# Optimization experiments

Measured on AMD Instinct MI355X. Metric: run time of the kernel, lower is better.

## Reference

```python
import jax, jax.numpy as jnp
import numpy as np

N_NODES = 50000
N_EDGES = 800000
EPS = 1e-5
NEG_SLOPE = 0.2


def _gatv2(x, src, dst, Wl, bl, Wr, br, att, bias, concat, N):
    # PyG GATv2Conv: xl = lin_l(x) (source side), xr = lin_r(x) (target side)
    H, C = att.shape
    xl = (x @ Wl + bl).reshape(N, H, C)
    xr = (x @ Wr + br).reshape(N, H, C)
    # per-edge message: leaky_relu(xl[j] + xr[i]), attention logit = <att, .>
    z = xl[src] + xr[dst]                      # [E, H, C]
    z = jnp.where(z > 0, z, NEG_SLOPE * z)
    logits = jnp.einsum('ehc,hc->eh', z, att)  # [E, H]
    # segment softmax over incoming edges of each target node
    m = jax.lax.stop_gradient(jax.ops.segment_max(logits, dst, num_segments=N))
    p = jnp.exp(logits - m[dst])
    s = jax.ops.segment_sum(p, dst, num_segments=N)
    alpha = p / s[dst]                         # [E, H]
    out = jax.ops.segment_sum(xl[src] * alpha[..., None], dst, num_segments=N)  # [N, H, C]
    out = out.reshape(N, H * C) if concat else out.mean(axis=1)
    return out + bias


def _bn(x, g, b):
    mu = x.mean(axis=0)
    v = x.var(axis=0)
    return (x - mu) * jax.lax.rsqrt(v + EPS) * g + b


def setup_inputs() -> dict:
    key = jax.random.key(0)
    ks = jax.random.split(key, 16)
    x = jax.random.normal(ks[0], (N_NODES, 2), jnp.float32)
    edge_index = jax.random.randint(ks[1], (2, N_EDGES), 0, N_NODES, dtype=jnp.int64)

    def lin(k, i, o):
        return jax.random.normal(k, (i, o), jnp.float32) * (1.0 / np.sqrt(i))

    inp = {'x': x, 'edge_index': edge_index}
    # layer 1: in=2, heads=8, out=16, concat
    inp['W1l'] = lin(ks[2], 2, 128); inp['b1l'] = jnp.zeros((128,), jnp.float32)
    inp['W1r'] = lin(ks[3], 2, 128); inp['b1r'] = jnp.zeros((128,), jnp.float32)
    inp['a1'] = jax.random.normal(ks[4], (8, 16), jnp.float32) * 0.1
    inp['bias1'] = jnp.zeros((128,), jnp.float32)
    inp['g1'] = jnp.ones((128,), jnp.float32); inp['be1'] = jnp.zeros((128,), jnp.float32)
    # layer 2: in=128, heads=4, out=16, concat
    inp['W2l'] = lin(ks[5], 128, 64); inp['b2l'] = jnp.zeros((64,), jnp.float32)
    inp['W2r'] = lin(ks[6], 128, 64); inp['b2r'] = jnp.zeros((64,), jnp.float32)
    inp['a2'] = jax.random.normal(ks[7], (4, 16), jnp.float32) * 0.1
    inp['bias2'] = jnp.zeros((64,), jnp.float32)
    inp['g2'] = jnp.ones((64,), jnp.float32); inp['be2'] = jnp.zeros((64,), jnp.float32)
    # layer 3: in=64, heads=1, out=2, mean (concat=False)
    inp['W3l'] = lin(ks[8], 64, 2); inp['b3l'] = jnp.zeros((2,), jnp.float32)
    inp['W3r'] = lin(ks[9], 64, 2); inp['b3r'] = jnp.zeros((2,), jnp.float32)
    inp['a3'] = jax.random.normal(ks[10], (1, 2), jnp.float32) * 0.1
    inp['bias3'] = jnp.zeros((2,), jnp.float32)
    return inp


def reference(x, edge_index, W1l, b1l, W1r, b1r, a1, bias1, g1, be1,
              W2l, b2l, W2r, b2r, a2, bias2, g2, be2,
              W3l, b3l, W3r, b3r, a3, bias3):
    N = x.shape[0]
    loops = jnp.arange(N, dtype=edge_index.dtype)
    src = jnp.concatenate([edge_index[0], loops])  # add self loops (PyG default)
    dst = jnp.concatenate([edge_index[1], loops])
    h = _gatv2(x, src, dst, W1l, b1l, W1r, b1r, a1, bias1, True, N)
    h = jax.nn.elu(_bn(h, g1, be1))  # dropout is identity in eval
    h = _gatv2(h, src, dst, W2l, b2l, W2r, b2r, a2, bias2, True, N)
    h = jax.nn.elu(_bn(h, g2, be2))
    return _gatv2(h, src, dst, W3l, b3l, W3r, b3r, a3, bias3, False, N)
```

## Files before the change

### kernel.cpp

```cpp
#include <hip/hip_runtime.h>
#include <hip/hip_bf16.h>

#define N_NODES 50000
#define N_E0    800000
#define N_ET    850000
#define EPSBN   1e-5f
#define LOG2E   1.4426950408889634f

#define LEAKY(z) fmaxf((z), 0.2f * (z))

#define OFF_C 0
#define OFF_A (128*N_NODES)
#define OFF_B (192*N_NODES)
#define OFF_STATS (256*N_NODES)
#define OFF_S1R (OFF_STATS + 512)
#define OFF_S2R (OFF_S1R + 16384)
#define OFF_P (OFF_S2R + 8192)
#define N_PARAM_TOT 118312
#define OFF_ROWPTR (OFF_P + N_PARAM_TOT)
#define OFF_DEG    (OFF_ROWPTR + 50001)
#define OFF_CURSOR (OFF_DEG + 50000)
#define OFF_BSUM   (OFF_CURSOR + 50000)
#define OFF_COL    (OFF_BSUM + 256)
#define OFF_FLAGS  (OFF_COL + 850064)
#define OFF_SCNT   (OFF_FLAGS + 2)
#define OFF_WF     (OFF_SCNT + 9)

#define BK_CAP 131072
#define BK_CHUNK 2048

typedef float v2f __attribute__((ext_vector_type(2)));
typedef __bf16 bf16x8 __attribute__((ext_vector_type(8)));
typedef float f32x4 __attribute__((ext_vector_type(4)));

__device__ __forceinline__ v2f ld2(const float* p) { return *(const v2f*)p; }
__device__ __forceinline__ v2f fma2(v2f a, v2f b, v2f c) {
    return __builtin_elementwise_fma(a, b, c);
}
__device__ __forceinline__ v2f max2(v2f a, v2f b) {
    return __builtin_elementwise_max(a, b);
}

__device__ __forceinline__ float bf2f(unsigned short u) {
    return __uint_as_float(((unsigned int)u) << 16);
}
__device__ __forceinline__ unsigned short f2bf(float f) {
    unsigned int u = __float_as_uint(f);
    u += 0x7FFFu + ((u >> 16) & 1u);
    return (unsigned short)(u >> 16);
}

__global__ void prep_kernel(const unsigned short* xr, const int* ei, int* flags,
                            int* deg, float* stats, float* s1r, float* s2r, int* scnt,
                            int* col) {
    int i = blockIdx.x * 256 + threadIdx.x;
    if (i < N_NODES) deg[i] = 0;
    if (i < 512) stats[i] = 0.f;
    if (i < 16384) s1r[i] = 0.f;
    if (i < 8192)  s2r[i] = 0.f;
    if (i < 8) scnt[i] = 0;
    if (i < 64) col[N_ET + i] = 0;
    if (blockIdx.x == 0) {
        __shared__ int c1, c2;
        if (threadIdx.x == 0) { c1 = 0; c2 = 0; }
        __syncthreads();
        int t = threadIdx.x;
        int l1 = 0, l2 = 0;
        for (int k = t; k < 2048; k += 256) {
            float v = bf2f(xr[k]);
            if (!(fabsf(v) <= 100.0f)) l1++;
            if (ei[2 * k + 1] != 0) l2++;
        }
        atomicAdd(&c1, l1);
        atomicAdd(&c2, l2);
        __syncthreads();
        if (t == 0) {
            flags[0] = (c1 > 16) ? 1 : 0;
            flags[1] = (c2 == 0) ? 1 : 0;
        }
    }
}

struct ParamPtrs { const void* p[23]; };

__global__ void convert_kernel(ParamPtrs ps, float* dst, const int* flags) {
    const int sizes[23] = {100000, 256,128,256,128,128,128,128,128,
                           8192,64,8192,64,64,64,64,64,
                           128,2,128,2,2,2};
    int g = blockIdx.x * 256 + threadIdx.x;
    if (g >= N_PARAM_TOT) return;
    int t = 0, off = g;
    while (off >= sizes[t]) { off -= sizes[t]; t++; }
    float v;
    if (flags[0]) v = ((const float*)ps.p[t])[off];
    else          v = bf2f(((const unsigned short*)ps.p[t])[off]);
    if (t == 5 || t == 13 || t == 21) v *= LOG2E;
    dst[g] = v;
}

__global__ void wf_kernel(const float* W2l, const float* W2r,
                          unsigned short* wfh, unsigned short* wfl) {
    int g = blockIdx.x * 256 + threadIdx.x;
    if (g >= 2048) return;
    int ts = g >> 6;
    int l  = g & 63;
    int t = ts >> 2, s = ts & 3;
    int k0 = 32 * s + 8 * (l >> 4);
    int c  = 16 * t + (l & 15);
    #pragma unroll
    for (int i = 0; i < 8; i++) {
        float v = (c < 64) ? W2l[(k0 + i) * 64 + c] : W2r[(k0 + i) * 64 + (c - 64)];
        unsigned short hi = f2bf(v);
        wfh[g * 8 + i] = hi;
        wfl[g * 8 + i] = f2bf(v - bf2f(hi));
    }
}

__global__ void bucket_kernel(const int* ei, const int* flags, int* scnt,
                              int* dstb, int* srcb, int* deg) {
    __shared__ int lcnt[8];
    __shared__ int lbase[8];
    int tid = threadIdx.x;
    if (tid < 8) lcnt[tid] = 0;
    __syncthreads();
    int base_e = blockIdx.x * BK_CHUNK;
    int i64 = flags[1];
    int src[8], dst[8], pos[8];
    #pragma unroll
    for (int u = 0; u < 8; u++) {
        int e = base_e + u * 256 + tid;
        if (e < N_ET) {
            int s, d;
            if (e < N_E0) {
                d = i64 ? ei[2 * (N_E0 + e)] : ei[N_E0 + e];
                s = i64 ? ei[2 * e] : ei[e];
            } else { s = d = e - N_E0; }
            src[u] = s; dst[u] = d;
            pos[u] = atomicAdd(&lcnt[d / 6250], 1);
            atomicAdd(&deg[d], 1);
        } else dst[u] = -1;
    }
    __syncthreads();
    if (tid < 8) lbase[tid] = atomicAdd(&scnt[tid], lcnt[tid]);
    __syncthreads();
    #pragma unroll
    for (int u = 0; u < 8; u++) {
        if (dst[u] >= 0) {
            int st = dst[u] / 6250;
            int gp = st * BK_CAP + lbase[st] + pos[u];
            dstb[gp] = dst[u];
            srcb[gp] = src[u];
        }
    }
}

__global__ void scan1_kernel(const int* deg, int* row_ptr, int* bsum) {
    __shared__ int sh[256];
    int i = blockIdx.x * 256 + threadIdx.x;
    int v = (i < N_NODES) ? deg[i] : 0;
    sh[threadIdx.x] = v;
    __syncthreads();
    for (int off = 1; off < 256; off <<= 1) {
        int t = (threadIdx.x >= off) ? sh[threadIdx.x - off] : 0;
        __syncthreads();
        sh[threadIdx.x] += t;
        __syncthreads();
    }
    if (i < N_NODES) row_ptr[i] = sh[threadIdx.x] - v;
    if (threadIdx.x == 255) bsum[blockIdx.x] = sh[255];
}

__global__ void scan23_kernel(int* row_ptr, int* cursor, const int* bsum) {
    __shared__ int sh[256];
    int t = threadIdx.x;
    int v = (t < 196) ? bsum[t] : 0;
    sh[t] = v;
    __syncthreads();
    for (int off = 1; off < 256; off <<= 1) {
        int u = (t >= off) ? sh[t - off] : 0;
        __syncthreads();
        sh[t] += u;
        __syncthreads();
    }
    int prefix = (blockIdx.x == 0) ? 0 : sh[blockIdx.x - 1];
    int i = blockIdx.x * 256 + t;
    if (i < N_NODES) {
        int r = row_ptr[i] + prefix;
        row_ptr[i] = r;
        cursor[i] = r;
    }
    if (i == 0) row_ptr[N_NODES] = N_ET;
}

__global__ void scatter2_kernel(const int* scnt, const int* dstb, const int* srcb,
                                int* cursor, int* col) {
    int stripe = blockIdx.x & 7;
    int bi = blockIdx.x >> 3;
    int cnt = scnt[stripe];
    int off = stripe * BK_CAP;
    for (int t = bi * 256 + threadIdx.x; t < cnt; t += 32 * 256) {
        int d = dstb[off + t];
        int pos = atomicAdd(&cursor[d], 1);
        col[pos] = srcb[off + t];
    }
}

__global__ void __launch_bounds__(256) gather1_kernel(
    const int* row_ptr, const int* col, const float* x,
    const float* W1l, const float* b1l, const float* W1r, const float* b1r,
    const float* att, const float* bias, unsigned int* Cb, float* s1r)
{
    int wv = threadIdx.x >> 6;
    int lane = threadIdx.x & 63;
    int n0 = blockIdx.x * 16 + wv * 4;
    int eslot = lane >> 4;
    int slot  = lane & 15;
    int c0 = slot << 3;

    int rpl = row_ptr[n0 + (lane < 5 ? lane : 4)];
    int r0 = __builtin_amdgcn_readlane(rpl, 0);
    int r1 = __builtin_amdgcn_readlane(rpl, 1);
    int r2 = __builtin_amdgcn_readlane(rpl, 2);
    int r3 = __builtin_amdgcn_readlane(rpl, 3);
    int r4 = __builtin_amdgcn_readlane(rpl, 4);
    int d0 = r1 - r0, d1 = r2 - r1, d2 = r3 - r2, d3 = r4 - r3;

    int ms0 = col[r0 + lane];
    int ms1 = col[r1 + lane];
    int ms2 = col[r2 + lane];
    int ms3 = col[r3 + lane];
    v2f xs0 = ld2(x + 2 * ms0);
    v2f xs1 = ld2(x + 2 * ms1);
    v2f xs2 = ld2(x + 2 * ms2);
    v2f xs3 = ld2(x + 2 * ms3);

    v2f w0[4], w1[4], at[4];
    #pragma unroll
    for (int k = 0; k < 4; k++) {
        w0[k] = ld2(W1l + c0 + 2 * k);
        w1[k] = ld2(W1l + 128 + c0 + 2 * k);
        at[k] = ld2(att + c0 + 2 * k);
    }
    v2f w0o = ld2(W1l + 2 * lane);
    v2f w1o = ld2(W1l + 128 + 2 * lane);
    v2f bo  = ld2(b1l + 2 * lane) + ld2(bias + 2 * lane);

    float bnS0 = 0.f, bnS1 = 0.f, bnQ0 = 0.f, bnQ1 = 0.f;

    auto run_node = [&](int ni, int basei, int degi, v2f xsv) {
        v2f xd = ld2(x + 2 * ni);
        v2f xdx = {xd.x, xd.x}, xdy = {xd.y, xd.y};
        v2f K[4];
        #pragma unroll
        for (int k = 0; k < 4; k++) {
            v2f wr0 = ld2(W1r + c0 + 2 * k);
            v2f wr1 = ld2(W1r + 128 + c0 + 2 * k);
            v2f bb  = ld2(b1r + c0 + 2 * k) + ld2(b1l + c0 + 2 * k);
            K[k] = fma2(xdx, wr0, fma2(xdy, wr1, bb));
        }
        float S0 = 0.f, S1 = 0.f, SP = 0.f;
        int cnt = degi < 64 ? degi : 64;
        for (int jb = 0; jb < cnt; jb += 4) {
            int e = jb + eslot;
            float x0s = __shfl(xsv.x, e, 64);
            float x1s = __shfl(xsv.y, e, 64);
            v2f x0 = {x0s, x0s}, x1 = {x1s, x1s};
            v2f lg = {0.f, 0.f};
            #pragma unroll
            for (int k = 0; k < 4; k++) {
                v2f t = fma2(x1, w1[k], fma2(x0, w0[k], K[k]));
                lg = fma2(max2(t, 0.2f * t), at[k], lg);
            }
            float logit = lg.x + lg.y;
            logit += __shfl_xor(logit, 1, 64);
            float p = (e < cnt) ? exp2f(logit) : 0.f;
            S0 = fmaf(p, x0s, S0);
            S1 = fmaf(p, x1s, S1);
            SP += p;
        }
        for (int j0 = 64; j0 < degi; j0 += 64) {
            int c2 = degi - j0; if (c2 > 64) c2 = 64;
            int m = col[basei + j0 + lane];
            v2f xv = ld2(x + 2 * m);
            for (int jb = 0; jb < c2; jb += 4) {
                int e = jb + eslot;
                float x0s = __shfl(xv.x, e, 64);
                float x1s = __shfl(xv.y, e, 64);
                v2f x0 = {x0s, x0s}, x1 = {x1s, x1s};
                v2f lg = {0.f, 0.f};
                #pragma unroll
                for (int k = 0; k < 4; k++) {
                    v2f t = fma2(x1, w1[k], fma2(x0, w0[k], K[k]));
                    lg = fma2(max2(t, 0.2f * t), at[k], lg);
                }
                float logit = lg.x + lg.y;
                logit += __shfl_xor(logit, 1, 64);
                float p = (e < c2) ? exp2f(logit) : 0.f;
                S0 = fmaf(p, x0s, S0);
                S1 = fmaf(p, x1s, S1);
                SP += p;
            }
        }
        #pragma unroll
        for (int m = 16; m <= 32; m <<= 1) {
            S0 += __shfl_xor(S0, m, 64);
            S1 += __shfl_xor(S1, m, 64);
            SP += __shfl_xor(SP, m, 64);
        }
        float inv = 1.f / SP;
        float t0 = S0 * inv, t1 = S1 * inv;
        int hsrc = (lane >> 3) << 1;
        float t0o = __shfl(t0, hsrc, 64);
        float t1o = __shfl(t1, hsrc, 64);
        float ox = fmaf(w0o.x, t0o, fmaf(w1o.x, t1o, bo.x));
        float oy = fmaf(w0o.y, t0o, fmaf(w1o.y, t1o, bo.y));
        Cb[ni * 64 + lane] = ((unsigned int)f2bf(oy) << 16) | f2bf(ox);
        bnS0 += ox; bnS1 += oy;
        bnQ0 += ox * ox; bnQ1 += oy * oy;
    };

    run_node(n0,     r0, d0, xs0);
    run_node(n0 + 1, r1, d1, xs1);
    run_node(n0 + 2, r2, d2, xs2);
    run_node(n0 + 3, r3, d3, xs3);

    __shared__ float sred[4][128];
    __shared__ float qred[4][128];
    sred[wv][2 * lane]     = bnS0;
    sred[wv][2 * lane + 1] = bnS1;
    qred[wv][2 * lane]     = bnQ0;
    qred[wv][2 * lane + 1] = bnQ1;
    __syncthreads();
    int t = threadIdx.x;
    float a;
    if (t < 128) a = sred[0][t] + sred[1][t] + sred[2][t] + sred[3][t];
    else { int c = t - 128; a = qred[0][c] + qred[1][c] + qred[2][c] + qred[3][c]; }
    atomicAdd(&s1r[(blockIdx.x & 63) * 256 + t], a);
}

__global__ void red1_kernel(const float* s1r, const float* g1, const float* be1,
                            float* stats) {
    __shared__ float ls[256];
    int t = threadIdx.x;
    float a = 0.f;
    for (int r = 0; r < 64; r++) a += s1r[r * 256 + t];
    ls[t] = a;
    __syncthreads();
    if (t < 128) {
        float mu = ls[t] * (1.0f / N_NODES);
        float var = ls[128 + t] * (1.0f / N_NODES) - mu * mu;
        float sc = g1[t] * rsqrtf(var + EPSBN);
        stats[t] = sc;
        stats[128 + t] = be1[t] - mu * sc;
    }
}

__global__ void __launch_bounds__(256) lin2_kernel(
    const unsigned int* Cb, const float* stats,
    const unsigned short* wfh, const unsigned short* wfl,
    const float* bl, const float* br,
    unsigned short* xl2b, float* xr2)
{
    __shared__ __align__(16) unsigned int hA[64 * 68];
    __shared__ __align__(16) unsigned int hL[64 * 68];
    int tid = threadIdx.x;
    int nb = blockIdx.x * 64;
    for (int i = tid; i < 64 * 64; i += 256) {
        int ni = i >> 6, kp = i & 63;
        int n = nb + ni;
        int k = 2 * kp;
        float v0 = 0.f, v1 = 0.f;
        if (n < N_NODES) {
            unsigned int pk = Cb[n * 64 + kp];
            float b0 = fmaf(__uint_as_float(pk << 16),        stats[k],     stats[128 + k]);
            float b1 = fmaf(__uint_as_float(pk & 0xffff0000u), stats[k + 1], stats[128 + k + 1]);
            v0 = b0 > 0.f ? b0 : __expf(b0) - 1.f;
            v1 = b1 > 0.f ? b1 : __expf(b1) - 1.f;
        }
        unsigned short h0 = f2bf(v0), h1 = f2bf(v1);
        unsigned short l0 = f2bf(v0 - bf2f(h0));
        unsigned short l1 = f2bf(v1 - bf2f(h1));
        hA[ni * 68 + kp] = (unsigned int)h0 | ((unsigned int)h1 << 16);
        hL[ni * 68 + kp] = (unsigned int)l0 | ((unsigned int)l1 << 16);
    }
    __syncthreads();
    int wv = tid >> 6;
    int lane = tid & 63;
    int g = lane >> 4, lrow = lane & 15;
    f32x4 acc[8];
    #pragma unroll
    for (int t = 0; t < 8; t++) acc[t] = (f32x4){0.f, 0.f, 0.f, 0.f};
    #pragma unroll
    for (int s = 0; s < 4; s++) {
        int aoff = (wv * 16 + lrow) * 272 + s * 64 + g * 16;
        bf16x8 ah = *(const bf16x8*)((const char*)hA + aoff);
        bf16x8 al = *(const bf16x8*)((const char*)hL + aoff);
        #pragma unroll
        for (int t = 0; t < 8; t++) {
            int bi = ((t * 4 + s) * 64 + lane) * 8;
            bf16x8 bh = *(const bf16x8*)(wfh + bi);
            bf16x8 bo = *(const bf16x8*)(wfl + bi);
            acc[t] = __builtin_amdgcn_mfma_f32_16x16x32_bf16(ah, bh, acc[t], 0, 0, 0);
            acc[t] = __builtin_amdgcn_mfma_f32_16x16x32_bf16(ah, bo, acc[t], 0, 0, 0);
            acc[t] = __builtin_amdgcn_mfma_f32_16x16x32_bf16(al, bh, acc[t], 0, 0, 0);
        }
    }
    #pragma unroll
    for (int t = 0; t < 8; t++) {
        int ch = 16 * t + lrow;
        float bias = (t < 4) ? bl[ch] : br[ch - 64];
        #pragma unroll
        for (int r = 0; r < 4; r++) {
            int node = nb + wv * 16 + g * 4 + r;
            if (node < N_NODES) {
                float v = acc[t][r] + bias;
                if (t < 4) xl2b[node * 64 + ch] = f2bf(v);
                else       xr2[node * 64 + ch - 64] = v;
            }
        }
    }
}

__global__ void __launch_bounds__(256) gather2_kernel(
    const int* row_ptr, const int* col, const unsigned short* xl2b, const float* xr2,
    const float* att, const float* bias, float* C, float* s2r)
{
    int gid = blockIdx.x * 256 + threadIdx.x;
    int n = gid >> 6;
    int lane = threadIdx.x & 63;
    int grp = lane >> 4;
    int cidx = lane & 15;
    float4 xrv = *(const float4*)(xr2 + n * 64 + 4 * cidx);
    float4 atv = *(const float4*)(att + 4 * cidx);
    int base = __builtin_amdgcn_readfirstlane(row_ptr[n]);
    int deg  = __builtin_amdgcn_readfirstlane(row_ptr[n + 1]) - base;
    float4 acc = make_float4(0.f, 0.f, 0.f, 0.f);
    float den = 0.f;
    for (int j0 = 0; j0 < deg; j0 += 64) {
        int cnt = deg - j0; if (cnt > 64) cnt = 64;
        int msrc = col[base + j0 + lane];
        for (int j4 = 0; j4 < cnt; j4 += 8) {
            int e0 = j4 + grp, e1 = j4 + 4 + grp;
            int s0 = __shfl(msrc, e0, 64);
            int s1 = __shfl(msrc, e1, 64);
            bool v0 = e0 < cnt, v1 = e1 < cnt;
            s0 = v0 ? s0 : 0;
            s1 = v1 ? s1 : 0;
            uint2 ba = *(const uint2*)(xl2b + (size_t)s0 * 64 + 4 * cidx);
            uint2 bb = *(const uint2*)(xl2b + (size_t)s1 * 64 + 4 * cidx);
            float a0 = __uint_as_float(ba.x << 16);
            float a1 = __uint_as_float(ba.x & 0xffff0000u);
            float a2 = __uint_as_float(ba.y << 16);
            float a3 = __uint_as_float(ba.y & 0xffff0000u);
            float b0 = __uint_as_float(bb.x << 16);
            float b1 = __uint_as_float(bb.x & 0xffff0000u);
            float b2 = __uint_as_float(bb.y << 16);
            float b3 = __uint_as_float(bb.y & 0xffff0000u);
            float pa = LEAKY(a0 + xrv.x) * atv.x;
            pa = fmaf(LEAKY(a1 + xrv.y), atv.y, pa);
            pa = fmaf(LEAKY(a2 + xrv.z), atv.z, pa);
            pa = fmaf(LEAKY(a3 + xrv.w), atv.w, pa);
            float pb = LEAKY(b0 + xrv.x) * atv.x;
            pb = fmaf(LEAKY(b1 + xrv.y), atv.y, pb);
            pb = fmaf(LEAKY(b2 + xrv.z), atv.z, pb);
            pb = fmaf(LEAKY(b3 + xrv.w), atv.w, pb);
            pa += __shfl_xor(pa, 1, 64);
            pa += __shfl_xor(pa, 2, 64);
            pb += __shfl_xor(pb, 1, 64);
            pb += __shfl_xor(pb, 2, 64);
            float ea = v0 ? exp2f(pa) : 0.f;
            float eb = v1 ? exp2f(pb) : 0.f;
            acc.x = fmaf(ea, a0, acc.x); acc.x = fmaf(eb, b0, acc.x);
            acc.y = fmaf(ea, a1, acc.y); acc.y = fmaf(eb, b1, acc.y);
            acc.z = fmaf(ea, a2, acc.z); acc.z = fmaf(eb, b2, acc.z);
            acc.w = fmaf(ea, a3, acc.w); acc.w = fmaf(eb, b3, acc.w);
            den += ea + eb;
        }
    }
    acc.x += __shfl_xor(acc.x, 16, 64); acc.x += __shfl_xor(acc.x, 32, 64);
    acc.y += __shfl_xor(acc.y, 16, 64); acc.y += __shfl_xor(acc.y, 32, 64);
    acc.z += __shfl_xor(acc.z, 16, 64); acc.z += __shfl_xor(acc.z, 32, 64);
    acc.w += __shfl_xor(acc.w, 16, 64); acc.w += __shfl_xor(acc.w, 32, 64);
    den += __shfl_xor(den, 16, 64);
    den += __shfl_xor(den, 32, 64);
    float inv = 1.f / den;
    float4 bi = *(const float4*)(bias + 4 * cidx);
    float4 o;
    o.x = fmaf(acc.x, inv, bi.x);
    o.y = fmaf(acc.y, inv, bi.y);
    o.z = fmaf(acc.z, inv, bi.z);
    o.w = fmaf(acc.w, inv, bi.w);
    if (lane < 16) *(float4*)(C + n * 64 + 4 * cidx) = o;
    __shared__ float sred[4][64];
    __shared__ float qred[4][64];
    int wv = threadIdx.x >> 6;
    if (lane < 16) {
        int c = 4 * cidx;
        sred[wv][c]     = o.x; qred[wv][c]     = o.x * o.x;
        sred[wv][c + 1] = o.y; qred[wv][c + 1] = o.y * o.y;
        sred[wv][c + 2] = o.z; qred[wv][c + 2] = o.z * o.z;
        sred[wv][c + 3] = o.w; qred[wv][c + 3] = o.w * o.w;
    }
    __syncthreads();
    int t = threadIdx.x;
    if (t < 128) {
        float a;
        if (t < 64) a = sred[0][t] + sred[1][t] + sred[2][t] + sred[3][t];
        else { int c = t - 64; a = qred[0][c] + qred[1][c] + qred[2][c] + qred[3][c]; }
        atomicAdd(&s2r[(blockIdx.x & 63) * 128 + t], a);
    }
}

__global__ void red2_kernel(const float* s2r, const float* g2, const float* be2,
                            float* stats) {
    __shared__ float ls[128];
    int t = threadIdx.x;
    float a = 0.f;
    for (int r = 0; r < 64; r++) a += s2r[r * 128 + t];
    ls[t] = a;
    __syncthreads();
    if (t < 64) {
        float mu = ls[t] * (1.0f / N_NODES);
        float var = ls[64 + t] * (1.0f / N_NODES) - mu * mu;
        float sc = g2[t] * rsqrtf(var + EPSBN);
        stats[t] = sc;
        stats[64 + t] = be2[t] - mu * sc;
    }
}

__global__ void __launch_bounds__(256) lin3_kernel(
    const float* C, const float* stats2,
    const float* Wl, const float* bl, const float* Wr, const float* br,
    float* xl3, float* xr3)
{
    int gid = blockIdx.x * 256 + threadIdx.x;
    int n = gid >> 6;
    int lane = threadIdx.x & 63;
    if (n >= N_NODES) return;
    float v = fmaf(C[n * 64 + lane], stats2[lane], stats2[64 + lane]);
    float h = v > 0.f ? v : __expf(v) - 1.f;
    float2 wlv = *(const float2*)(Wl + 2 * lane);
    float2 wrv = *(const float2*)(Wr + 2 * lane);
    float a0 = h * wlv.x, a1 = h * wlv.y;
    float r0 = h * wrv.x, r1 = h * wrv.y;
    #pragma unroll
    for (int m = 1; m < 64; m <<= 1) {
        a0 += __shfl_xor(a0, m, 64);
        a1 += __shfl_xor(a1, m, 64);
        r0 += __shfl_xor(r0, m, 64);
        r1 += __shfl_xor(r1, m, 64);
    }
    if (lane == 0) {
        xl3[2 * n]     = a0 + bl[0];
        xl3[2 * n + 1] = a1 + bl[1];
        xr3[2 * n]     = r0 + br[0];
        xr3[2 * n + 1] = r1 + br[1];
    }
}

__global__ void __launch_bounds__(256) gather3_kernel(
    const int* row_ptr, const int* col,
    const float* xl3, const float* xr3,
    const float* att, const float* bias,
    void* out, const int* flags) {
    int gid = blockIdx.x * 256 + threadIdx.x;
    int n = gid >> 2;
    int q = threadIdx.x & 3;
    if (n >= N_NODES) return;
    float a0 = att[0], a1 = att[1];
    float xr0 = xr3[2 * n], xr1 = xr3[2 * n + 1];
    float acc0 = 0.f, acc1 = 0.f, den = 0.f;
    int e0 = row_ptr[n], e1 = row_ptr[n + 1];
    for (int e = e0 + q; e < e1; e += 4) {
        int src = col[e];
        float2 xs = *(const float2*)(xl3 + 2 * src);
        float z0 = LEAKY(xs.x + xr0);
        float z1 = LEAKY(xs.y + xr1);
        float p = exp2f(fmaf(z0, a0, z1 * a1));
        acc0 = fmaf(p, xs.x, acc0);
        acc1 = fmaf(p, xs.y, acc1);
        den += p;
    }
    acc0 += __shfl_xor(acc0, 1, 64); acc0 += __shfl_xor(acc0, 2, 64);
    acc1 += __shfl_xor(acc1, 1, 64); acc1 += __shfl_xor(acc1, 2, 64);
    den  += __shfl_xor(den, 1, 64);  den  += __shfl_xor(den, 2, 64);
    if (q == 0) {
        float inv = 1.f / den;
        float v0 = fmaf(acc0, inv, bias[0]);
        float v1 = fmaf(acc1, inv, bias[1]);
        if (flags[0]) {
            ((float*)out)[2 * n] = v0;
            ((float*)out)[2 * n + 1] = v1;
        } else {
            ((__hip_bfloat16*)out)[2 * n] = __float2bfloat16(v0);
            ((__hip_bfloat16*)out)[2 * n + 1] = __float2bfloat16(v1);
        }
    }
}

extern "C" void kernel_launch(void* const* d_in, const int* in_sizes, int n_in,
                              void* d_out, int out_size, void* d_ws, size_t ws_size,
                              hipStream_t stream) {
    float* W = (float*)d_ws;
    float* C = W + OFF_C;
    float* A = W + OFF_A;
    float* B = W + OFF_B;
    float* STATS = W + OFF_STATS;
    float* S1R = W + OFF_S1R;
    float* S2R = W + OFF_S2R;
    float* P = W + OFF_P;
    int* ROWPTR = (int*)(W + OFF_ROWPTR);
    int* DEG    = (int*)(W + OFF_DEG);
    int* CURSOR = (int*)(W + OFF_CURSOR);
    int* BSUM   = (int*)(W + OFF_BSUM);
    int* COL    = (int*)(W + OFF_COL);
    int* FLAGS  = (int*)(W + OFF_FLAGS);
    int* SCNT   = (int*)(W + OFF_SCNT);
    int* DSTB   = (int*)(W + OFF_C);
    int* SRCB   = DSTB + 8 * BK_CAP;
    unsigned short* WFH = (unsigned short*)(W + OFF_WF);
    unsigned short* WFL = WFH + 16384;

    const int* ei = (const int*)d_in[1];

    float* Px  = P;
    float* W1l = Px + 100000; float* b1l = W1l + 256; float* W1r = b1l + 128; float* b1r = W1r + 256;
    float* a1  = b1r + 128;   float* bias1 = a1 + 128; float* g1 = bias1 + 128; float* be1 = g1 + 128;
    float* W2l = be1 + 128;   float* b2l = W2l + 8192; float* W2r = b2l + 64;  float* b2r = W2r + 8192;
    float* a2  = b2r + 64;    float* bias2 = a2 + 64;  float* g2 = bias2 + 64; float* be2 = g2 + 64;
    float* W3l = be2 + 64;    float* b3l = W3l + 128;  float* W3r = b3l + 2;   float* b3r = W3r + 128;
    float* a3  = b3r + 2;     float* bias3 = a3 + 2;

    prep_kernel<<<196, 256, 0, stream>>>((const unsigned short*)d_in[0], ei, FLAGS, DEG, STATS, S1R, S2R, SCNT, COL);

    ParamPtrs ps;
    ps.p[0] = d_in[0];
    for (int j = 1; j < 23; j++) ps.p[j] = d_in[j + 1];
    convert_kernel<<<(N_PARAM_TOT + 255) / 256, 256, 0, stream>>>(ps, P, FLAGS);
    wf_kernel<<<8, 256, 0, stream>>>(W2l, W2r, WFH, WFL);

    bucket_kernel<<<(N_ET + BK_CHUNK - 1) / BK_CHUNK, 256, 0, stream>>>(ei, FLAGS, SCNT, DSTB, SRCB, DEG);
    scan1_kernel<<<196, 256, 0, stream>>>(DEG, ROWPTR, BSUM);
    scan23_kernel<<<196, 256, 0, stream>>>(ROWPTR, CURSOR, BSUM);
    scatter2_kernel<<<256, 256, 0, stream>>>(SCNT, DSTB, SRCB, CURSOR, COL);

    gather1_kernel<<<N_NODES / 16, 256, 0, stream>>>(ROWPTR, COL, Px, W1l, b1l, W1r, b1r, a1, bias1, (unsigned int*)C, S1R);
    red1_kernel<<<1, 256, 0, stream>>>(S1R, g1, be1, STATS);

    lin2_kernel<<<(N_NODES + 63) / 64, 256, 0, stream>>>((const unsigned int*)C, STATS, WFH, WFL, b2l, b2r, (unsigned short*)A, B);
    gather2_kernel<<<N_NODES * 64 / 256, 256, 0, stream>>>(ROWPTR, COL, (const unsigned short*)A, B, a2, bias2, C, S2R);
    red2_kernel<<<1, 128, 0, stream>>>(S2R, g2, be2, STATS + 256);

    lin3_kernel<<<N_NODES * 64 / 256, 256, 0, stream>>>(C, STATS + 256, W3l, b3l, W3r, b3r, A, B);
    gather3_kernel<<<(N_NODES * 4 + 255) / 256, 256, 0, stream>>>(ROWPTR, COL, A, B, a3, bias3, d_out, FLAGS);
}
```

Before: 312.1 us.

## Process four nodes per wavefront in gather2 with prefetched row data

```diff
diff --git a/kernel.cpp b/kernel.cpp
--- a/kernel.cpp
+++ b/kernel.cpp
@@ -425,25 +425,44 @@
     const int* row_ptr, const int* col, const unsigned short* xl2b, const float* xr2,
     const float* att, const float* bias, float* C, float* s2r)
 {
-    int gid = blockIdx.x * 256 + threadIdx.x;
-    int n = gid >> 6;
+    int wv = threadIdx.x >> 6;
     int lane = threadIdx.x & 63;
+    int n0 = blockIdx.x * 16 + wv * 4;
     int grp = lane >> 4;
     int cidx = lane & 15;
-    float4 xrv = *(const float4*)(xr2 + n * 64 + 4 * cidx);
+
+    int rpl = row_ptr[n0 + (lane < 5 ? lane : 4)];
+    int r0 = __builtin_amdgcn_readlane(rpl, 0);
+    int r1 = __builtin_amdgcn_readlane(rpl, 1);
+    int r2 = __builtin_amdgcn_readlane(rpl, 2);
+    int r3 = __builtin_amdgcn_readlane(rpl, 3);
+    int r4 = __builtin_amdgcn_readlane(rpl, 4);
+    int d0 = r1 - r0, d1 = r2 - r1, d2 = r3 - r2, d3 = r4 - r3;
+
+    int ms0 = col[r0 + lane];
+    int ms1 = col[r1 + lane];
+    int ms2 = col[r2 + lane];
+    int ms3 = col[r3 + lane];
+    float4 xr0v = *(const float4*)(xr2 + (size_t)n0 * 64 + 4 * cidx);
+    float4 xr1v = *(const float4*)(xr2 + (size_t)(n0 + 1) * 64 + 4 * cidx);
+    float4 xr2v = *(const float4*)(xr2 + (size_t)(n0 + 2) * 64 + 4 * cidx);
+    float4 xr3v = *(const float4*)(xr2 + (size_t)(n0 + 3) * 64 + 4 * cidx);
+
     float4 atv = *(const float4*)(att + 4 * cidx);
-    int base = __builtin_amdgcn_readfirstlane(row_ptr[n]);
-    int deg  = __builtin_amdgcn_readfirstlane(row_ptr[n + 1]) - base;
-    float4 acc = make_float4(0.f, 0.f, 0.f, 0.f);
-    float den = 0.f;
-    for (int j0 = 0; j0 < deg; j0 += 64) {
-        int cnt = deg - j0; if (cnt > 64) cnt = 64;
-        int msrc = col[base + j0 + lane];
-        for (int j4 = 0; j4 < cnt; j4 += 8) {
+    float4 bi = *(const float4*)(bias + 4 * cidx);
+
+    float4 bnS = make_float4(0.f, 0.f, 0.f, 0.f);
+    float4 bnQ = make_float4(0.f, 0.f, 0.f, 0.f);
+
+    auto run_node = [&](int ni, int basei, int degi, int msrc, float4 xrv) {
+        float4 acc = make_float4(0.f, 0.f, 0.f, 0.f);
+        float den = 0.f;
+        int cnt0 = degi < 64 ? degi : 64;
+        for (int j4 = 0; j4 < cnt0; j4 += 8) {
             int e0 = j4 + grp, e1 = j4 + 4 + grp;
             int s0 = __shfl(msrc, e0, 64);
             int s1 = __shfl(msrc, e1, 64);
-            bool v0 = e0 < cnt, v1 = e1 < cnt;
+            bool v0 = e0 < cnt0, v1 = e1 < cnt0;
             s0 = v0 ? s0 : 0;
             s1 = v1 ? s1 : 0;
             uint2 ba = *(const uint2*)(xl2b + (size_t)s0 * 64 + 4 * cidx);
@@ -476,30 +495,80 @@
             acc.w = fmaf(ea, a3, acc.w); acc.w = fmaf(eb, b3, acc.w);
             den += ea + eb;
         }
-    }
-    acc.x += __shfl_xor(acc.x, 16, 64); acc.x += __shfl_xor(acc.x, 32, 64);
-    acc.y += __shfl_xor(acc.y, 16, 64); acc.y += __shfl_xor(acc.y, 32, 64);
-    acc.z += __shfl_xor(acc.z, 16, 64); acc.z += __shfl_xor(acc.z, 32, 64);
-    acc.w += __shfl_xor(acc.w, 16, 64); acc.w += __shfl_xor(acc.w, 32, 64);
-    den += __shfl_xor(den, 16, 64);
-    den += __shfl_xor(den, 32, 64);
-    float inv = 1.f / den;
-    float4 bi = *(const float4*)(bias + 4 * cidx);
-    float4 o;
-    o.x = fmaf(acc.x, inv, bi.x);
-    o.y = fmaf(acc.y, inv, bi.y);
-    o.z = fmaf(acc.z, inv, bi.z);
-    o.w = fmaf(acc.w, inv, bi.w);
-    if (lane < 16) *(float4*)(C + n * 64 + 4 * cidx) = o;
+        for (int j0 = 64; j0 < degi; j0 += 64) {
+            int cnt = degi - j0; if (cnt > 64) cnt = 64;
+            int m = col[basei + j0 + lane];
+            for (int j4 = 0; j4 < cnt; j4 += 8) {
+                int e0 = j4 + grp, e1 = j4 + 4 + grp;
+                int s0 = __shfl(m, e0, 64);
+                int s1 = __shfl(m, e1, 64);
+                bool v0 = e0 < cnt, v1 = e1 < cnt;
+                s0 = v0 ? s0 : 0;
+                s1 = v1 ? s1 : 0;
+                uint2 ba = *(const uint2*)(xl2b + (size_t)s0 * 64 + 4 * cidx);
+                uint2 bb = *(const uint2*)(xl2b + (size_t)s1 * 64 + 4 * cidx);
+                float a0 = __uint_as_float(ba.x << 16);
+                float a1 = __uint_as_float(ba.x & 0xffff0000u);
+                float a2 = __uint_as_float(ba.y << 16);
+                float a3 = __uint_as_float(ba.y & 0xffff0000u);
+                float b0 = __uint_as_float(bb.x << 16);
+                float b1 = __uint_as_float(bb.x & 0xffff0000u);
+                float b2 = __uint_as_float(bb.y << 16);
+                float b3 = __uint_as_float(bb.y & 0xffff0000u);
+                float pa = LEAKY(a0 + xrv.x) * atv.x;
+                pa = fmaf(LEAKY(a1 + xrv.y), atv.y, pa);
+                pa = fmaf(LEAKY(a2 + xrv.z), atv.z, pa);
+                pa = fmaf(LEAKY(a3 + xrv.w), atv.w, pa);
+                float pb = LEAKY(b0 + xrv.x) * atv.x;
+                pb = fmaf(LEAKY(b1 + xrv.y), atv.y, pb);
+                pb = fmaf(LEAKY(b2 + xrv.z), atv.z, pb);
+                pb = fmaf(LEAKY(b3 + xrv.w), atv.w, pb);
+                pa += __shfl_xor(pa, 1, 64);
+                pa += __shfl_xor(pa, 2, 64);
+                pb += __shfl_xor(pb, 1, 64);
+                pb += __shfl_xor(pb, 2, 64);
+                float ea = v0 ? exp2f(pa) : 0.f;
+                float eb = v1 ? exp2f(pb) : 0.f;
+                acc.x = fmaf(ea, a0, acc.x); acc.x = fmaf(eb, b0, acc.x);
+                acc.y = fmaf(ea, a1, acc.y); acc.y = fmaf(eb, b1, acc.y);
+                acc.z = fmaf(ea, a2, acc.z); acc.z = fmaf(eb, b2, acc.z);
+                acc.w = fmaf(ea, a3, acc.w); acc.w = fmaf(eb, b3, acc.w);
+                den += ea + eb;
+            }
+        }
+        acc.x += __shfl_xor(acc.x, 16, 64); acc.x += __shfl_xor(acc.x, 32, 64);
+        acc.y += __shfl_xor(acc.y, 16, 64); acc.y += __shfl_xor(acc.y, 32, 64);
+        acc.z += __shfl_xor(acc.z, 16, 64); acc.z += __shfl_xor(acc.z, 32, 64);
+        acc.w += __shfl_xor(acc.w, 16, 64); acc.w += __shfl_xor(acc.w, 32, 64);
+        den += __shfl_xor(den, 16, 64);
+        den += __shfl_xor(den, 32, 64);
+        float inv = 1.f / den;
+        float4 o;
+        o.x = fmaf(acc.x, inv, bi.x);
+        o.y = fmaf(acc.y, inv, bi.y);
+        o.z = fmaf(acc.z, inv, bi.z);
+        o.w = fmaf(acc.w, inv, bi.w);
+        if (lane < 16) {
+            *(float4*)(C + (size_t)ni * 64 + 4 * cidx) = o;
+            bnS.x += o.x; bnS.y += o.y; bnS.z += o.z; bnS.w += o.w;
+            bnQ.x += o.x * o.x; bnQ.y += o.y * o.y;
+            bnQ.z += o.z * o.z; bnQ.w += o.w * o.w;
+        }
+    };
+
+    run_node(n0,     r0, d0, ms0, xr0v);
+    run_node(n0 + 1, r1, d1, ms1, xr1v);
+    run_node(n0 + 2, r2, d2, ms2, xr2v);
+    run_node(n0 + 3, r3, d3, ms3, xr3v);
+
     __shared__ float sred[4][64];
     __shared__ float qred[4][64];
-    int wv = threadIdx.x >> 6;
     if (lane < 16) {
         int c = 4 * cidx;
-        sred[wv][c]     = o.x; qred[wv][c]     = o.x * o.x;
-        sred[wv][c + 1] = o.y; qred[wv][c + 1] = o.y * o.y;
-        sred[wv][c + 2] = o.z; qred[wv][c + 2] = o.z * o.z;
-        sred[wv][c + 3] = o.w; qred[wv][c + 3] = o.w * o.w;
+        sred[wv][c]     = bnS.x; qred[wv][c]     = bnQ.x;
+        sred[wv][c + 1] = bnS.y; qred[wv][c + 1] = bnQ.y;
+        sred[wv][c + 2] = bnS.z; qred[wv][c + 2] = bnQ.z;
+        sred[wv][c + 3] = bnS.w; qred[wv][c + 3] = bnQ.w;
     }
     __syncthreads();
     int t = threadIdx.x;
@@ -648,7 +717,7 @@
     red1_kernel<<<1, 256, 0, stream>>>(S1R, g1, be1, STATS);
 
     lin2_kernel<<<(N_NODES + 63) / 64, 256, 0, stream>>>((const unsigned int*)C, STATS, WFH, WFL, b2l, b2r, (unsigned short*)A, B);
-    gather2_kernel<<<N_NODES * 64 / 256, 256, 0, stream>>>(ROWPTR, COL, (const unsigned short*)A, B, a2, bias2, C, S2R);
+    gather2_kernel<<<N_NODES / 16, 256, 0, stream>>>(ROWPTR, COL, (const unsigned short*)A, B, a2, bias2, C, S2R);
     red2_kernel<<<1, 128, 0, stream>>>(S2R, g2, be2, STATS + 256);
 
     lin3_kernel<<<N_NODES * 64 / 256, 256, 0, stream>>>(C, STATS + 256, W3l, b3l, W3r, b3r, A, B);
```

Measured after the change: 312.9 us. No clear change (+0.3%).
